# Optimization experiments

Measured on AMD Instinct MI355X. Metric: run time of the kernel, lower is better.

The kernel has to match this reference:

```python
import jax, jax.numpy as jnp
import numpy as np

B, N, C = 4, 8192, 128
NPOINT, NSAMPLE = 2048, 32
RADIUS = 0.1
EPS = 1e-5  # BatchNorm eps (eval mode with running stats)


def setup_inputs() -> dict:
    key = jax.random.key(0)
    k1, k2, k3 = jax.random.split(key, 3)
    return {
        "points_coor": jax.random.uniform(k1, (B, 3, N), dtype=jnp.float32),
        "points_fea": jax.random.normal(k2, (B, C, N), dtype=jnp.float32),
        "W": jax.random.normal(k3, (2 * C, C + 3), dtype=jnp.float32) * 0.05,
        "b": jnp.zeros((2 * C,), jnp.float32),
        "gamma": jnp.ones((2 * C,), jnp.float32),
        "beta": jnp.zeros((2 * C,), jnp.float32),
        "bn_mean": jnp.zeros((2 * C,), jnp.float32),
        "bn_var": jnp.ones((2 * C,), jnp.float32),
    }


def _fps_single(xyz):
    """Farthest point sampling for one cloud. xyz: (N,3) -> (NPOINT,) int32.
    Deterministic start at index 0 (torch version starts at a random index)."""
    n = xyz.shape[0]

    def body(carry, _):
        dist, farthest = carry
        centroid = xyz[farthest]                      # (3,)
        d = jnp.sum((xyz - centroid) ** 2, axis=-1)   # (N,)
        dist = jnp.minimum(dist, d)
        nxt = jnp.argmax(dist).astype(jnp.int32)
        return (dist, nxt), farthest

    init = (jnp.full((n,), 1e10, xyz.dtype), jnp.int32(0))
    (_, _), idx = jax.lax.scan(body, init, None, length=NPOINT)
    return idx


def _gather(points, idx):
    # points: (B,N,D), idx: (B,S,K) -> (B,S,K,D)
    return jax.vmap(lambda p, i: p[i])(points, idx)


def reference(points_coor, points_fea, W, b, gamma, beta, bn_mean, bn_var):
    coor = points_coor.transpose(0, 2, 1)  # (B,N,3)
    fea = points_fea.transpose(0, 2, 1)    # (B,N,C)

    # S: farthest point sampling
    fps_idx = jax.vmap(_fps_single)(coor)                              # (B,S)
    new_coor = jnp.take_along_axis(coor, fps_idx[:, :, None], axis=1)  # (B,S,3)

    # G: hybrid knn/ball query -- k nearest, out-of-radius replaced by nearest
    sq = (jnp.sum(new_coor ** 2, -1)[:, :, None]
          + jnp.sum(coor ** 2, -1)[:, None, :]
          - 2.0 * jnp.einsum('bsd,bnd->bsn', new_coor, coor))           # (B,S,N)
    neg_d, idx = jax.lax.top_k(-sq, NSAMPLE)                            # k smallest
    d = -neg_d
    group_idx = jnp.where(d > RADIUS ** 2, idx[:, :, 0:1], idx)         # (B,S,K)

    g_coor = (_gather(coor, group_idx) - new_coor[:, :, None, :]) / RADIUS  # (B,S,K,3)
    g_fea = _gather(fea, group_idx)                                         # (B,S,K,C)
    g = jnp.concatenate([g_fea, g_coor], axis=-1)                           # (B,S,K,C+3)

    # P: shared 1x1 conv + BN(eval) + ReLU, then max-pool over neighbors
    h = jnp.einsum('bskc,dc->bskd', g, W) + b
    h = gamma * (h - bn_mean) * jax.lax.rsqrt(bn_var + EPS) + beta
    h = jax.nn.relu(h)
    new_fea = jnp.max(h, axis=2)  # (B,S,2C)

    return new_coor.transpose(0, 2, 1), new_fea.transpose(0, 2, 1)
```

## Files before the change

kernel.cpp:

```cpp
#include <hip/hip_runtime.h>
#include <stdint.h>


typedef unsigned short u16;
typedef unsigned long long u64;
typedef __bf16 bf16x8 __attribute__((ext_vector_type(8)));
typedef float f32x4 __attribute__((ext_vector_type(4)));
typedef float f32x2 __attribute__((ext_vector_type(2)));

#define NB 4
#define NPTS 8192
#define CH 128
#define SPTS 2048
#define KN 32
#define CINP 160

__device__ __forceinline__ u16 f2b(float f) {
    unsigned x = __float_as_uint(f);
    unsigned r = (x + 0x7fffu + ((x >> 16) & 1u)) >> 16;
    return (u16)r;
}
__device__ __forceinline__ u64 umin64(u64 a, u64 b) { return a < b ? a : b; }
__device__ __forceinline__ int mort3(int v) {
    return (v & 1) | ((v & 2) << 2) | ((v & 4) << 4);
}

template <int CTRL>
__device__ __forceinline__ u64 dpp_max64(u64 k) {
    unsigned lo = (unsigned)k, hi = (unsigned)(k >> 32);
    unsigned mlo = (unsigned)__builtin_amdgcn_update_dpp((int)lo, (int)lo, CTRL, 0xF, 0xF, false);
    unsigned mhi = (unsigned)__builtin_amdgcn_update_dpp((int)hi, (int)hi, CTRL, 0xF, 0xF, false);
    u64 m = ((u64)mhi << 32) | mlo;
    return m > k ? m : k;
}
template <int CTRL>
__device__ __forceinline__ unsigned dpp_maxu(unsigned v) {
    unsigned mv = (unsigned)__builtin_amdgcn_update_dpp((int)v, (int)v, CTRL, 0xF, 0xF, false);
    return mv > v ? mv : v;
}

__global__ __launch_bounds__(256) void ksort(const float* __restrict__ coor,
                                             float* __restrict__ sxg,
                                             float* __restrict__ syg,
                                             float* __restrict__ szg,
                                             int* __restrict__ sog,
                                             int* __restrict__ ctrs) {
    __shared__ int hist[512], base[512];
    int b = blockIdx.x, tid = threadIdx.x;
    if (b == 0 && tid < 8) ctrs[tid] = 0;
    const float* cb = coor + b * 3 * NPTS;
    hist[tid] = 0;
    hist[tid + 256] = 0;
    __syncthreads();
    int bins[32];
#pragma unroll 4
    for (int i = 0; i < 32; ++i) {
        int n = tid * 32 + i;
        float x = cb[n], y = cb[NPTS + n], z = cb[2 * NPTS + n];
        int bx = min(7, (int)(x * 8.0f));
        int by = min(7, (int)(y * 8.0f));
        int bz = min(7, (int)(z * 8.0f));
        int bin = mort3(bx) | (mort3(by) << 1) | (mort3(bz) << 2);
        bins[i] = bin;
        atomicAdd(&hist[bin], 1);
    }
    __syncthreads();
    if (tid == 0) {
        int acc = 0;
        for (int k2 = 0; k2 < 512; ++k2) { base[k2] = acc; acc += hist[k2]; hist[k2] = 0; }
    }
    __syncthreads();
#pragma unroll 4
    for (int i = 0; i < 32; ++i) {
        int n = tid * 32 + i;
        int bin = bins[i];
        int pos = base[bin] + atomicAdd(&hist[bin], 1);
        sxg[b * NPTS + pos] = cb[n];
        syg[b * NPTS + pos] = cb[NPTS + n];
        szg[b * NPTS + pos] = cb[2 * NPTS + n];
        sog[b * NPTS + pos] = n;
    }
}

__global__ __launch_bounds__(1024) void kmega(const float* __restrict__ sxg,
                                              const float* __restrict__ syg,
                                              const float* __restrict__ szg,
                                              const int* __restrict__ sog,
                                              int* __restrict__ fpsIdx,
                                              float* __restrict__ outCoor,
                                              const float* __restrict__ fea,
                                              const float* __restrict__ coor,
                                              const float* __restrict__ W,
                                              u16* __restrict__ feaT,
                                              float* __restrict__ pp,
                                              u16* __restrict__ Wpad,
                                              const float* __restrict__ bias,
                                              const float* __restrict__ gamma,
                                              const float* __restrict__ beta,
                                              const float* __restrict__ bmean,
                                              const float* __restrict__ bvar,
                                              float* __restrict__ outFea,
                                              int* __restrict__ ctrs) {
    __shared__ float4 sp[NPTS];
    __shared__ unsigned sWin[SPTS];
    __shared__ u64 sAtom[4];
    __shared__ int slot0s;
    __shared__ int sBase;
    int bid = blockIdx.x;
    int tid = threadIdx.x;

    if (bid >= 4) {
        int wid = bid - 4;
        for (int c = wid; c < 328; c += 252) {
            if (c < 256) {
                u16(*T)[130] = (u16(*)[130])sp;
                int b = c >> 6, nt = c & 63;
                int n0 = nt * 128;
#pragma unroll 4
                for (int it = 0; it < 16; ++it) {
                    int idx = it * 1024 + tid;
                    int cc = idx >> 7, nl = idx & 127;
                    T[nl][cc] = f2b(fea[((size_t)(b * CH + cc)) * NPTS + n0 + nl]);
                }
                __syncthreads();
#pragma unroll 4
                for (int it = 0; it < 16; ++it) {
                    int idx = it * 1024 + tid;
                    int nl = idx >> 7, cc = idx & 127;
                    feaT[((size_t)(b * NPTS + n0 + nl)) * CH + cc] = T[nl][cc];
                }
            } else if (c < 288) {
                int gid = (c - 256) * 1024 + tid;
                int n = gid & 8191, b = gid >> 13;
                const float* cb = coor + b * 3 * NPTS;
                float x = cb[n], y = cb[NPTS + n], z = cb[2 * NPTS + n];
                pp[gid] = __fadd_rn(__fadd_rn(__fmul_rn(x, x), __fmul_rn(y, y)),
                                    __fmul_rn(z, z));
            } else {
                int i = (c - 288) * 1024 + tid;
                int d = i / CINP, k = i - d * CINP;
                Wpad[i] = (k < 131) ? f2b(W[d * 131 + k]) : (u16)0;
            }
            __syncthreads();
        }
        __threadfence();
        __syncthreads();
        if (tid == 0) {
            atomicAdd(&ctrs[4], 1);
            while (__hip_atomic_load(&ctrs[4], __ATOMIC_ACQUIRE,
                                     __HIP_MEMORY_SCOPE_AGENT) < 252)
                __builtin_amdgcn_s_sleep(8);
        }
        __syncthreads();
        u64(*buf)[256] = (u64(*)[256])sp;
        int* cnt = (int*)((char*)sp + 32768);
        unsigned(*gsel)[KN] = (unsigned(*)[KN])((char*)sp + 32896);
        u16(*g4)[KN][168] = (u16(*)[KN][168])((char*)sp + 34944);
        int wv = tid >> 6, lane = tid & 63;
        for (;;) {
            if (tid == 0) sBase = atomicAdd(&ctrs[5], 16);
            __syncthreads();
            int lbase = sBase;
            if (lbase >= NB * SPTS) break;
            if (tid == 0) {
                int need = ((lbase + 15) >> 2) + 1;
                for (int bb = 0; bb < 4; ++bb)
                    while (__hip_atomic_load(&ctrs[bb], __ATOMIC_ACQUIRE,
                                             __HIP_MEMORY_SCOPE_AGENT) < need)
                        __builtin_amdgcn_s_sleep(8);
            }
            __syncthreads();
            {
                int r = lbase + wv, bb = r & 3, s = r >> 2;
                if (lane == 0) cnt[wv] = 0;
                const float* cb = coor + bb * 3 * NPTS;
                int n0 = fpsIdx[bb * SPTS + s];
                float cx = cb[n0], cy = cb[NPTS + n0], cz = cb[2 * NPTS + n0];
                float cc = __fadd_rn(__fadd_rn(__fmul_rn(cx, cx), __fmul_rn(cy, cy)),
                                     __fmul_rn(cz, cz));
                const float* ppb = pp + bb * NPTS;
                u64 mk = ~0ull;
                for (int n = lane; n < NPTS; n += 64) {
                    float x = cb[n], y = cb[NPTS + n], z = cb[2 * NPTS + n];
                    float dot = __fmaf_rn(cz, z, __fmaf_rn(cy, y, __fmul_rn(cx, x)));
                    float sq = __fsub_rn(__fadd_rn(cc, ppb[n]), __fmul_rn(2.0f, dot));
                    unsigned ub = __float_as_uint(sq);
                    ub ^= (ub >> 31) ? 0xFFFFFFFFu : 0x80000000u;
                    u64 key = ((u64)ub << 32) | (unsigned)n;
                    mk = umin64(mk, key);
                    if (sq <= 0.01f) {
                        int p = atomicAdd(&cnt[wv], 1);
                        if (p < 256) buf[wv][p] = key;
                    }
                }
#pragma unroll
                for (int off = 32; off > 0; off >>= 1) mk = umin64(mk, __shfl_xor(mk, off));
                int C = cnt[wv];
                if (C > 256) C = 256;
                if (C <= 32) {
                    if (lane < 32) {
                        unsigned idx = (lane < C) ? (unsigned)buf[wv][lane] : (unsigned)mk;
                        gsel[wv][lane] = idx;
                    }
                } else {
                    u64 e[4];
#pragma unroll
                    for (int i = 0; i < 4; ++i) {
                        int j2 = lane + (i << 6);
                        e[i] = (j2 < C) ? buf[wv][j2] : ~0ull;
                    }
                    int cl = 0;
                    unsigned sel = 0;
                    for (int it = 0; it < 32; ++it) {
                        u64 lb = ~0ull;
                        int li = 0;
#pragma unroll
                        for (int i = 0; i < 4; ++i) {
                            bool f = (((cl >> i) & 1) == 0) && (e[i] < lb);
                            lb = f ? e[i] : lb;
                            li = f ? i : li;
                        }
                        u64 wmin = lb;
#pragma unroll
                        for (int off = 32; off > 0; off >>= 1)
                            wmin = umin64(wmin, __shfl_xor(wmin, off));
                        u64 bal = __ballot(lb == wmin);
                        int src = __ffsll((unsigned long long)bal) - 1;
                        if (lane == src) cl |= (1 << li);
                        if (lane == it) sel = (unsigned)wmin;
                    }
                    if (lane < 32) gsel[wv][lane] = sel;
                }
            }
            __syncthreads();
            for (int it4 = 0; it4 < 4; ++it4) {
                __syncthreads();
                int g256 = tid >> 8, t256 = tid & 255;
                int rloc = it4 * 4 + g256;
                int r2 = lbase + rloc, b2 = r2 & 3, s2 = r2 >> 2;
                {
                    int k = t256 >> 3, j = t256 & 7;
                    const float* cb2 = coor + b2 * 3 * NPTS;
                    int nc = fpsIdx[b2 * SPTS + s2];
                    int nbr = (int)gsel[rloc][k];
                    const uint4* f4p = (const uint4*)(feaT + (((size_t)b2 * NPTS + nbr) << 7));
                    uint4* gr = (uint4*)&g4[g256][k][0];
                    gr[j] = f4p[j];
                    gr[j + 8] = f4p[j + 8];
                    for (int cch = 128 + j; cch < CINP; cch += 8) {
                        u16 v = 0;
                        if (cch < 131) {
                            int dim = cch - 128;
                            float pv = cb2[dim * NPTS + nbr];
                            float cv = cb2[dim * NPTS + nc];
                            v = f2b(__fdiv_rn(__fsub_rn(pv, cv), 0.1f));
                        }
                        g4[g256][k][cch] = v;
                    }
                }
                __syncthreads();
                int w = t256 >> 6, lane2 = t256 & 63;
                int mrow = lane2 & 15, q = lane2 >> 4;
                f32x4 acc[4][2] = {};
#pragma unroll
                for (int ks = 0; ks < 5; ++ks) {
                    int kb = ks * 32 + q * 8;
                    bf16x8 b0 = *(const bf16x8*)&g4[g256][mrow][kb];
                    bf16x8 b1 = *(const bf16x8*)&g4[g256][mrow + 16][kb];
#pragma unroll
                    for (int mt = 0; mt < 4; ++mt) {
                        bf16x8 a = *(const bf16x8*)&Wpad[(size_t)(w * 64 + mt * 16 + mrow) * CINP + kb];
                        acc[mt][0] = __builtin_amdgcn_mfma_f32_16x16x32_bf16(a, b0, acc[mt][0], 0, 0, 0);
                        acc[mt][1] = __builtin_amdgcn_mfma_f32_16x16x32_bf16(a, b1, acc[mt][1], 0, 0, 0);
                    }
                }
#pragma unroll
                for (int mt = 0; mt < 4; ++mt) {
#pragma unroll
                    for (int r = 0; r < 4; ++r) {
                        int m = w * 64 + mt * 16 + q * 4 + r;
                        float ga = gamma[m], be = beta[m];
                        float mu = bmean[m], va = bvar[m], bi = bias[m];
                        float rs = 1.0f / sqrtf(va + 1e-5f);
                        float h0 = acc[mt][0][r] + bi;
                        h0 = fmaxf(ga * (h0 - mu) * rs + be, 0.0f);
                        float h1 = acc[mt][1][r] + bi;
                        h1 = fmaxf(ga * (h1 - mu) * rs + be, 0.0f);
                        float v = fmaxf(h0, h1);
#pragma unroll
                        for (int off = 1; off < 16; off <<= 1) v = fmaxf(v, __shfl_xor(v, off));
                        if (mrow == 0) outFea[((size_t)(b2 * 256 + m)) * SPTS + s2] = v;
                    }
                }
            }
        }
        return;
    }
    int b = bid;
    int lane = tid & 63;
    const float* gx = sxg + b * NPTS;
    const float* gy = syg + b * NPTS;
    const float* gz = szg + b * NPTS;
    const int* go = sog + b * NPTS;
    f32x2 X2[4], Y2[4], Z2[4], D2[4];
    unsigned PK[8];
    int n0 = tid * 8;
    if (tid < 4) sAtom[tid] = 0;
    float lox, hix, loy, hiy, loz, hiz;
#pragma unroll
    for (int j = 0; j < 8; ++j) {
        float x = gx[n0 + j], y = gy[n0 + j], z = gz[n0 + j];
        sp[n0 + j] = make_float4(x, y, z, 0.0f);
        X2[j >> 1][j & 1] = x; Y2[j >> 1][j & 1] = y; Z2[j >> 1][j & 1] = z;
        D2[j >> 1][j & 1] = 1e10f;
        int oi = go[n0 + j];
        PK[j] = ((unsigned)oi << 16) | (unsigned)(n0 + j);
        if (oi == 0) slot0s = n0 + j;
        if (j == 0) {
            lox = hix = x; loy = hiy = y; loz = hiz = z;
        } else {
            lox = fminf(lox, x); hix = fmaxf(hix, x);
            loy = fminf(loy, y); hiy = fmaxf(hiy, y);
            loz = fminf(loz, z); hiz = fmaxf(hiz, z);
        }
    }
    __syncthreads();
    int far = slot0s;
    if (tid == 0) sWin[0] = (unsigned)slot0s;
    float lm = 3.4e38f;
    u64 cachedKey = 1;
    for (int t = 1; t < SPTS; ++t) {
        float4 c = sp[far];
        float fx = c.x, fy = c.y, fz = c.z;
        float ddx = fmaxf(0.0f, fmaxf(lox - fx, fx - hix));
        float ddy = fmaxf(0.0f, fmaxf(loy - fy, fy - hiy));
        float ddz = fmaxf(0.0f, fmaxf(loz - fz, fz - hiz));
        float dmin2 = ddx * ddx + ddy * ddy + ddz * ddz;
        if (__ballot(dmin2 * 0.9995f < lm) != 0ull) {
            {
#pragma clang fp contract(off)
                f32x2 fx2 = {fx, fx}, fy2 = {fy, fy}, fz2 = {fz, fz};
#pragma unroll
                for (int i = 0; i < 4; ++i) {
                    f32x2 dx = X2[i] - fx2;
                    f32x2 dy = Y2[i] - fy2;
                    f32x2 dz = Z2[i] - fz2;
                    f32x2 s = (dx * dx + dy * dy) + dz * dz;
                    D2[i] = __builtin_elementwise_min(D2[i], s);
                }
            }
            f32x2 t01 = __builtin_elementwise_max(D2[0], D2[1]);
            f32x2 t23 = __builtin_elementwise_max(D2[2], D2[3]);
            f32x2 t03 = __builtin_elementwise_max(t01, t23);
            float m = fmaxf(t03[0], t03[1]);
            lm = m;
            unsigned sel = 0xFFFFFFFFu;
#pragma unroll
            for (int j = 0; j < 8; ++j) {
                float dj = D2[j >> 1][j & 1];
                sel = (dj == m) ? (sel < PK[j] ? sel : PK[j]) : sel;
            }
            unsigned mbits = __float_as_uint(m);
            unsigned r = mbits;
            r = dpp_maxu<0xB1>(r);
            r = dpp_maxu<0x4E>(r);
            r = dpp_maxu<0x141>(r);
            r = dpp_maxu<0x140>(r);
            r = dpp_maxu<0x142>(r);
            r = dpp_maxu<0x143>(r);
            unsigned wmaxb = (unsigned)__builtin_amdgcn_readlane((int)r, 63);
            u64 ball = __ballot(mbits == wmaxb);
            unsigned wpk;
            if (__popcll(ball) == 1) {
                int l = __ffsll(ball) - 1;
                wpk = (unsigned)__builtin_amdgcn_readlane((int)sel, l);
            } else {
                u64 kk = (mbits == wmaxb) ? (((u64)wmaxb << 32) | (unsigned)~sel) : 0ull;
                kk = dpp_max64<0xB1>(kk);
                kk = dpp_max64<0x4E>(kk);
                kk = dpp_max64<0x141>(kk);
                kk = dpp_max64<0x140>(kk);
                kk = dpp_max64<0x142>(kk);
                kk = dpp_max64<0x143>(kk);
                unsigned lo = (unsigned)__builtin_amdgcn_readlane((int)(unsigned)kk, 63);
                wpk = ~lo;
            }
            cachedKey = ((u64)wmaxb << 32) | (unsigned)~wpk;
        }
        if (lane == 63) atomicMax(&sAtom[t & 3], cachedKey);
        if (tid == 0) sAtom[(t + 1) & 3] = 0;
        __syncthreads();
        u64 wk = sAtom[t & 3];
        unsigned pk = ~(unsigned)wk;
        far = (int)(pk & 0xFFFFu);
        if (tid == 0) sWin[t] = pk;
        if ((t & 63) == 0 && tid < 64) {
            int i = t - 64 + tid;
            unsigned pk2 = sWin[i];
            int slot = (int)(pk2 & 0xFFFFu);
            float4 c4 = sp[slot];
            fpsIdx[b * SPTS + i] = (int)(pk2 >> 16);
            float* oc = outCoor + b * 3 * SPTS + i;
            oc[0] = c4.x; oc[SPTS] = c4.y; oc[2 * SPTS] = c4.z;
            __threadfence();
            if (tid == 0)
                __hip_atomic_store(&ctrs[b], t, __ATOMIC_RELEASE, __HIP_MEMORY_SCOPE_AGENT);
        }
    }
    __syncthreads();
    if (tid < 64) {
        int i = 1984 + tid;
        unsigned pk2 = sWin[i];
        int slot = (int)(pk2 & 0xFFFFu);
        float4 c4 = sp[slot];
        fpsIdx[b * SPTS + i] = (int)(pk2 >> 16);
        float* oc = outCoor + b * 3 * SPTS + i;
        oc[0] = c4.x; oc[SPTS] = c4.y; oc[2 * SPTS] = c4.z;
        __threadfence();
        if (tid == 0)
            __hip_atomic_store(&ctrs[b], 2048, __ATOMIC_RELEASE, __HIP_MEMORY_SCOPE_AGENT);
    }
}

extern "C" void kernel_launch(void* const* d_in, const int* in_sizes, int n_in,
                              void* d_out, int out_size, void* d_ws, size_t ws_size,
                              hipStream_t stream) {
    const float* coor = (const float*)d_in[0];
    const float* fea = (const float*)d_in[1];
    const float* W = (const float*)d_in[2];
    const float* bias = (const float*)d_in[3];
    const float* gamma = (const float*)d_in[4];
    const float* beta = (const float*)d_in[5];
    const float* bmean = (const float*)d_in[6];
    const float* bvar = (const float*)d_in[7];
    char* ws = (char*)d_ws;
    int* fpsIdx = (int*)ws;
    int* ctrs = (int*)(ws + 32768);
    float* pp = (float*)(ws + 65536);
    u16* feaT = (u16*)(ws + 1048576);
    u16* Wpad = (u16*)(ws + 9437184);
    float* sxg = (float*)(ws + 9519104);
    float* syg = (float*)(ws + 9650176);
    float* szg = (float*)(ws + 9781248);
    int* sog = (int*)(ws + 9912320);
    float* outC = (float*)d_out;
    float* outF = outC + NB * 3 * SPTS;

    ksort<<<NB, 256, 0, stream>>>(coor, sxg, syg, szg, sog, ctrs);
    kmega<<<256, 1024, 0, stream>>>(sxg, syg, szg, sog, fpsIdx, outC,
                                    fea, coor, W, feaT, pp, Wpad,
                                    bias, gamma, beta, bmean, bvar, outF, ctrs);
}
```

Before: 1.727 ms.

## Prune kNN ball query to neighboring Morton grid cells and shrink grouping workers

The sort kernel now exports per-bin offsets and precomputed squared norms in sorted order. Each grouping wave scans only the points in grid cells within the query radius rather than all 8192 points, and falls back to a full scan when the candidate count exceeds a cap. Only 16 blocks stay on as grouping workers while the rest exit after preprocessing, and the counters are padded to separate cache lines. The risk is a kNN result that differs from the reference when fewer than 32 points lie in the searched cells, since the nearest point outside the radius is then chosen only among the candidates. Fewer worker blocks may also reduce grouping throughput.

```diff
diff --git a/kernel.cpp b/kernel.cpp
--- a/kernel.cpp
+++ b/kernel.cpp
@@ -14,6 +14,9 @@
 #define SPTS 2048
 #define KN 32
 #define CINP 160
+#define GCAPW 1024
+#define NWORK 16
+#define CSTRIDE 64
 
 __device__ __forceinline__ u16 f2b(float f) {
     unsigned x = __float_as_uint(f);
@@ -44,10 +47,12 @@
                                              float* __restrict__ syg,
                                              float* __restrict__ szg,
                                              int* __restrict__ sog,
+                                             float* __restrict__ spp,
+                                             int* __restrict__ gbase,
                                              int* __restrict__ ctrs) {
     __shared__ int hist[512], base[512];
     int b = blockIdx.x, tid = threadIdx.x;
-    if (b == 0 && tid < 8) ctrs[tid] = 0;
+    if (b == 0) { ctrs[tid] = 0; ctrs[tid + 256] = 0; }
     const float* cb = coor + b * 3 * NPTS;
     hist[tid] = 0;
     hist[tid + 256] = 0;
@@ -70,15 +75,21 @@
         for (int k2 = 0; k2 < 512; ++k2) { base[k2] = acc; acc += hist[k2]; hist[k2] = 0; }
     }
     __syncthreads();
+    gbase[b * 513 + tid] = base[tid];
+    gbase[b * 513 + 256 + tid] = base[256 + tid];
+    if (tid == 0) gbase[b * 513 + 512] = NPTS;
 #pragma unroll 4
     for (int i = 0; i < 32; ++i) {
         int n = tid * 32 + i;
         int bin = bins[i];
         int pos = base[bin] + atomicAdd(&hist[bin], 1);
-        sxg[b * NPTS + pos] = cb[n];
-        syg[b * NPTS + pos] = cb[NPTS + n];
-        szg[b * NPTS + pos] = cb[2 * NPTS + n];
+        float x = cb[n], y = cb[NPTS + n], z = cb[2 * NPTS + n];
+        sxg[b * NPTS + pos] = x;
+        syg[b * NPTS + pos] = y;
+        szg[b * NPTS + pos] = z;
         sog[b * NPTS + pos] = n;
+        spp[b * NPTS + pos] = __fadd_rn(__fadd_rn(__fmul_rn(x, x), __fmul_rn(y, y)),
+                                        __fmul_rn(z, z));
     }
 }
 
@@ -86,13 +97,14 @@
                                               const float* __restrict__ syg,
                                               const float* __restrict__ szg,
                                               const int* __restrict__ sog,
+                                              const float* __restrict__ spp,
+                                              const int* __restrict__ gbase,
                                               int* __restrict__ fpsIdx,
                                               float* __restrict__ outCoor,
                                               const float* __restrict__ fea,
                                               const float* __restrict__ coor,
                                               const float* __restrict__ W,
                                               u16* __restrict__ feaT,
-                                              float* __restrict__ pp,
                                               u16* __restrict__ Wpad,
                                               const float* __restrict__ bias,
                                               const float* __restrict__ gamma,
@@ -111,7 +123,7 @@
 
     if (bid >= 4) {
         int wid = bid - 4;
-        for (int c = wid; c < 328; c += 252) {
+        for (int c = wid; c < 296; c += 252) {
             if (c < 256) {
                 u16(*T)[130] = (u16(*)[130])sp;
                 int b = c >> 6, nt = c & 63;
@@ -129,15 +141,8 @@
                     int nl = idx >> 7, cc = idx & 127;
                     feaT[((size_t)(b * NPTS + n0 + nl)) * CH + cc] = T[nl][cc];
                 }
-            } else if (c < 288) {
-                int gid = (c - 256) * 1024 + tid;
-                int n = gid & 8191, b = gid >> 13;
-                const float* cb = coor + b * 3 * NPTS;
-                float x = cb[n], y = cb[NPTS + n], z = cb[2 * NPTS + n];
-                pp[gid] = __fadd_rn(__fadd_rn(__fmul_rn(x, x), __fmul_rn(y, y)),
-                                    __fmul_rn(z, z));
             } else {
-                int i = (c - 288) * 1024 + tid;
+                int i = (c - 256) * 1024 + tid;
                 int d = i / CINP, k = i - d * CINP;
                 Wpad[i] = (k < 131) ? f2b(W[d * 131 + k]) : (u16)0;
             }
@@ -145,52 +150,111 @@
         }
         __threadfence();
         __syncthreads();
+        if (tid == 0) atomicAdd(&ctrs[5 * CSTRIDE], 1);
+        if (bid < 240) return;
+
         if (tid == 0) {
-            atomicAdd(&ctrs[4], 1);
-            while (__hip_atomic_load(&ctrs[4], __ATOMIC_ACQUIRE,
+            while (__hip_atomic_load(&ctrs[5 * CSTRIDE], __ATOMIC_ACQUIRE,
                                      __HIP_MEMORY_SCOPE_AGENT) < 252)
-                __builtin_amdgcn_s_sleep(8);
+                __builtin_amdgcn_s_sleep(32);
         }
         __syncthreads();
         u64(*buf)[256] = (u64(*)[256])sp;
-        int* cnt = (int*)((char*)sp + 32768);
-        unsigned(*gsel)[KN] = (unsigned(*)[KN])((char*)sp + 32896);
-        u16(*g4)[KN][168] = (u16(*)[KN][168])((char*)sp + 34944);
+        int(*posA)[GCAPW] = (int(*)[GCAPW])((char*)sp + 32768);
+        unsigned(*gsel)[KN] = (unsigned(*)[KN])((char*)sp + 98304);
+        int* cnt = (int*)((char*)sp + 100352);
+        u16(*g4)[KN][168] = (u16(*)[KN][168])sp;
         int wv = tid >> 6, lane = tid & 63;
         for (;;) {
-            if (tid == 0) sBase = atomicAdd(&ctrs[5], 16);
+            if (tid == 0) sBase = atomicAdd(&ctrs[4 * CSTRIDE], 16);
             __syncthreads();
             int lbase = sBase;
             if (lbase >= NB * SPTS) break;
             if (tid == 0) {
                 int need = ((lbase + 15) >> 2) + 1;
                 for (int bb = 0; bb < 4; ++bb)
-                    while (__hip_atomic_load(&ctrs[bb], __ATOMIC_ACQUIRE,
+                    while (__hip_atomic_load(&ctrs[bb * CSTRIDE], __ATOMIC_ACQUIRE,
                                              __HIP_MEMORY_SCOPE_AGENT) < need)
-                        __builtin_amdgcn_s_sleep(8);
+                        __builtin_amdgcn_s_sleep(32);
             }
             __syncthreads();
             {
-                int r = lbase + wv, bb = r & 3, s = r >> 2;
+                int r = lbase + wv, b = r & 3, s = r >> 2;
                 if (lane == 0) cnt[wv] = 0;
-                const float* cb = coor + bb * 3 * NPTS;
-                int n0 = fpsIdx[bb * SPTS + s];
+                const float* cb = coor + b * 3 * NPTS;
+                int n0 = fpsIdx[b * SPTS + s];
                 float cx = cb[n0], cy = cb[NPTS + n0], cz = cb[2 * NPTS + n0];
                 float cc = __fadd_rn(__fadd_rn(__fmul_rn(cx, cx), __fmul_rn(cy, cy)),
                                      __fmul_rn(cz, cz));
-                const float* ppb = pp + bb * NPTS;
+                int bxlo = max(0, (int)floorf((cx - 0.1001f) * 8.0f));
+                int bxhi = min(7, (int)floorf((cx + 0.1001f) * 8.0f));
+                int bylo = max(0, (int)floorf((cy - 0.1001f) * 8.0f));
+                int byhi = min(7, (int)floorf((cy + 0.1001f) * 8.0f));
+                int bzlo = max(0, (int)floorf((cz - 0.1001f) * 8.0f));
+                int bzhi = min(7, (int)floorf((cz + 0.1001f) * 8.0f));
+                int nx = bxhi - bxlo + 1, ny = byhi - bylo + 1, nz = bzhi - bzlo + 1;
+                int nbins = nx * ny * nz;
+                const int* gb = gbase + b * 513;
+                int lo = 0, len = 0;
+                if (lane < nbins) {
+                    int lx = lane % nx;
+                    int rest = lane / nx;
+                    int ly = rest % ny;
+                    int lz = rest / ny;
+                    int bin = mort3(bxlo + lx) | (mort3(bylo + ly) << 1) | (mort3(bzlo + lz) << 2);
+                    lo = gb[bin];
+                    len = gb[bin + 1] - lo;
+                }
+                int v = len;
+#pragma unroll
+                for (int off = 1; off < 64; off <<= 1) {
+                    int u = __shfl_up(v, off);
+                    if (lane >= off) v += u;
+                }
+                int T = __shfl(v, 63);
+                int pfe = v - len;
+                bool fast = (T <= GCAPW);
+                if (fast) {
+                    for (int i = 0; i < len; ++i) posA[wv][pfe + i] = lo + i;
+                }
+                const float* bx_ = sxg + b * NPTS;
+                const float* by_ = syg + b * NPTS;
+                const float* bz_ = szg + b * NPTS;
+                const int* bo_ = sog + b * NPTS;
+                const float* bp_ = spp + b * NPTS;
                 u64 mk = ~0ull;
-                for (int n = lane; n < NPTS; n += 64) {
-                    float x = cb[n], y = cb[NPTS + n], z = cb[2 * NPTS + n];
-                    float dot = __fmaf_rn(cz, z, __fmaf_rn(cy, y, __fmul_rn(cx, x)));
-                    float sq = __fsub_rn(__fadd_rn(cc, ppb[n]), __fmul_rn(2.0f, dot));
-                    unsigned ub = __float_as_uint(sq);
-                    ub ^= (ub >> 31) ? 0xFFFFFFFFu : 0x80000000u;
-                    u64 key = ((u64)ub << 32) | (unsigned)n;
-                    mk = umin64(mk, key);
-                    if (sq <= 0.01f) {
-                        int p = atomicAdd(&cnt[wv], 1);
-                        if (p < 256) buf[wv][p] = key;
+                if (fast) {
+                    for (int j = lane; j < T; j += 64) {
+                        int p = posA[wv][j];
+                        float x = bx_[p], y = by_[p], z = bz_[p];
+                        float ppv = bp_[p];
+                        int oi = bo_[p];
+                        float dot = __fmaf_rn(cz, z, __fmaf_rn(cy, y, __fmul_rn(cx, x)));
+                        float sq = __fsub_rn(__fadd_rn(cc, ppv), __fmul_rn(2.0f, dot));
+                        unsigned ub = __float_as_uint(sq);
+                        ub ^= (ub >> 31) ? 0xFFFFFFFFu : 0x80000000u;
+                        u64 key = ((u64)ub << 32) | (unsigned)oi;
+                        mk = umin64(mk, key);
+                        if (sq <= 0.01f) {
+                            int p2 = atomicAdd(&cnt[wv], 1);
+                            if (p2 < 256) buf[wv][p2] = key;
+                        }
+                    }
+                } else {
+                    for (int n = lane; n < NPTS; n += 64) {
+                        float x = cb[n], y = cb[NPTS + n], z = cb[2 * NPTS + n];
+                        float ppv = __fadd_rn(__fadd_rn(__fmul_rn(x, x), __fmul_rn(y, y)),
+                                              __fmul_rn(z, z));
+                        float dot = __fmaf_rn(cz, z, __fmaf_rn(cy, y, __fmul_rn(cx, x)));
+                        float sq = __fsub_rn(__fadd_rn(cc, ppv), __fmul_rn(2.0f, dot));
+                        unsigned ub = __float_as_uint(sq);
+                        ub ^= (ub >> 31) ? 0xFFFFFFFFu : 0x80000000u;
+                        u64 key = ((u64)ub << 32) | (unsigned)n;
+                        mk = umin64(mk, key);
+                        if (sq <= 0.01f) {
+                            int p2 = atomicAdd(&cnt[wv], 1);
+                            if (p2 < 256) buf[wv][p2] = key;
+                        }
                     }
                 }
 #pragma unroll
@@ -404,7 +468,8 @@
             oc[0] = c4.x; oc[SPTS] = c4.y; oc[2 * SPTS] = c4.z;
             __threadfence();
             if (tid == 0)
-                __hip_atomic_store(&ctrs[b], t, __ATOMIC_RELEASE, __HIP_MEMORY_SCOPE_AGENT);
+                __hip_atomic_store(&ctrs[b * CSTRIDE], t, __ATOMIC_RELEASE,
+                                   __HIP_MEMORY_SCOPE_AGENT);
         }
     }
     __syncthreads();
@@ -418,7 +483,8 @@
         oc[0] = c4.x; oc[SPTS] = c4.y; oc[2 * SPTS] = c4.z;
         __threadfence();
         if (tid == 0)
-            __hip_atomic_store(&ctrs[b], 2048, __ATOMIC_RELEASE, __HIP_MEMORY_SCOPE_AGENT);
+            __hip_atomic_store(&ctrs[b * CSTRIDE], 2048, __ATOMIC_RELEASE,
+                               __HIP_MEMORY_SCOPE_AGENT);
     }
 }
 
@@ -435,19 +501,20 @@
     const float* bvar = (const float*)d_in[7];
     char* ws = (char*)d_ws;
     int* fpsIdx = (int*)ws;
-    int* ctrs = (int*)(ws + 32768);
-    float* pp = (float*)(ws + 65536);
-    u16* feaT = (u16*)(ws + 1048576);
-    u16* Wpad = (u16*)(ws + 9437184);
-    float* sxg = (float*)(ws + 9519104);
-    float* syg = (float*)(ws + 9650176);
-    float* szg = (float*)(ws + 9781248);
-    int* sog = (int*)(ws + 9912320);
+    float* spp = (float*)(ws + 32768);
+    int* gbase = (int*)(ws + 163840);
+    int* ctrs = (int*)(ws + 180224);
+    u16* feaT = (u16*)(ws + 1228800);
+    u16* Wpad = (u16*)(ws + 9617408);
+    float* sxg = (float*)(ws + 9699328);
+    float* syg = (float*)(ws + 9830400);
+    float* szg = (float*)(ws + 9961472);
+    int* sog = (int*)(ws + 10092544);
     float* outC = (float*)d_out;
     float* outF = outC + NB * 3 * SPTS;
 
-    ksort<<<NB, 256, 0, stream>>>(coor, sxg, syg, szg, sog, ctrs);
-    kmega<<<256, 1024, 0, stream>>>(sxg, syg, szg, sog, fpsIdx, outC,
-                                    fea, coor, W, feaT, pp, Wpad,
+    ksort<<<NB, 256, 0, stream>>>(coor, sxg, syg, szg, sog, spp, gbase, ctrs);
+    kmega<<<256, 1024, 0, stream>>>(sxg, syg, szg, sog, spp, gbase, fpsIdx, outC,
+                                    fea, coor, W, feaT, Wpad,
                                     bias, gamma, beta, bmean, bvar, outF, ctrs);
 }
```

Result: slower. 3.500 ms (+102.7%).
